# Performance work log

Hardware: AMD Instinct MI355X
Metric: run time of the kernel (lower is better)

## Reference

```python
import jax, jax.numpy as jnp
import numpy as np

N_NODES = 100000
N_EDGES = 1600000
N_CLASS = 45


def gcn_conv(x, W, b, src, dst, ew, n):
    # PyG GCNConv: add self-loops (weight 1), symmetric deg^-1/2 normalization,
    # linear transform, scatter-add aggregation into targets, then bias.
    loops = jnp.arange(n, dtype=src.dtype)
    s = jnp.concatenate([src, loops])
    d = jnp.concatenate([dst, loops])
    w = jnp.concatenate([ew, jnp.ones((n,), ew.dtype)])
    deg = jax.ops.segment_sum(w, d, num_segments=n)          # in-degree (weighted)
    dis = jnp.where(deg > 0, 1.0 / jnp.sqrt(deg), 0.0)      # deg^-1/2, 0 where deg==0
    norm = dis[s] * w * dis[d]                               # [E+n]
    h = x @ W                                                # [n, out]
    out = jax.ops.segment_sum(h[s] * norm[:, None], d, num_segments=n)
    return out + b


def setup_inputs() -> dict:
    key = jax.random.key(0)
    ks = jax.random.split(key, 6)
    x = jax.random.normal(ks[0], (N_NODES, N_CLASS), dtype=jnp.float32)
    edge_src = jax.random.randint(ks[1], (N_EDGES,), 0, N_NODES, dtype=jnp.int64 if jax.config.jax_enable_x64 else jnp.int32).astype(jnp.int32)
    edge_dst = jax.random.randint(ks[2], (N_EDGES,), 0, N_NODES, dtype=jnp.int64 if jax.config.jax_enable_x64 else jnp.int32).astype(jnp.int32)
    edge_w = jax.random.uniform(ks[3], (N_EDGES,), dtype=jnp.float32)
    W1 = jax.random.normal(ks[4], (N_CLASS, 32), dtype=jnp.float32) / np.sqrt(N_CLASS)
    b1 = jnp.zeros((32,), dtype=jnp.float32)
    W2 = jax.random.normal(ks[5], (32, 128), dtype=jnp.float32) / np.sqrt(32.0)
    b2 = jnp.zeros((128,), dtype=jnp.float32)
    return {"x": x, "edge_src": edge_src, "edge_dst": edge_dst, "edge_w": edge_w,
            "W1": W1, "b1": b1, "W2": W2, "b2": b2}


def reference(x, edge_src, edge_dst, edge_w, W1, b1, W2, b2):
    n = x.shape[0]
    h = jnp.tanh(gcn_conv(x, W1, b1, edge_src, edge_dst, edge_w, n))
    return gcn_conv(h, W2, b2, edge_src, edge_dst, edge_w, n)
```

## Files before the change

kernel.cpp:

```cpp
#include <hip/hip_runtime.h>
#include <hip/hip_fp16.h>
#include <math.h>

static constexpr int TPB = 256;
static constexpr int NPB_SHIFT = 8;
static constexpr int BCAP = 5120;
static constexpr int HCAP = 2816;
static constexpr int CSTRIDE = 2 * HCAP;
static constexpr int PCHUNK = 4096;
static constexpr int PF = 16;

__device__ __forceinline__ int p_src(unsigned p) { return (int)(p >> 15); }
__device__ __forceinline__ float p_w(unsigned p) {
  return __half2float(__ushort_as_half((unsigned short)(p & 0x7FFFu)));
}

struct h2x4 { __half2 a, b, c, d; };

__device__ __forceinline__ __half2 shfl_h2(__half2 v, int mask) {
  int b = *reinterpret_cast<int*>(&v);
  int r = __shfl_xor(b, mask, 64);
  return *reinterpret_cast<__half2*>(&r);
}

__global__ void k_partition(const int* __restrict__ src, const int* __restrict__ dst,
                            const float* __restrict__ ew, int* __restrict__ bkcnt,
                            unsigned* __restrict__ ppk, unsigned char* __restrict__ pld,
                            int E, int NB) {
  __shared__ int lh[512];
  __shared__ int lbase[512];
  __shared__ int lcur[512];
  int tid = threadIdx.x;
  long long e0 = (long long)blockIdx.x * PCHUNK;
  int d[PCHUNK / TPB];
  unsigned pk[PCHUNK / TPB];
  for (int t = tid; t < NB; t += TPB) { lh[t] = 0; lcur[t] = 0; }
  __syncthreads();
#pragma unroll
  for (int r = 0; r < PCHUNK / TPB; ++r) {
    long long e = e0 + (long long)r * TPB + tid;
    if (e < E) {
      d[r] = dst[e];
      pk[r] = ((unsigned)src[e] << 15) |
              ((unsigned)__half_as_ushort(__float2half(ew[e])) & 0x7FFFu);
      atomicAdd(&lh[d[r] >> NPB_SHIFT], 1);
    } else {
      d[r] = -1;
    }
  }
  __syncthreads();
  for (int t = tid; t < NB; t += TPB)
    lbase[t] = lh[t] ? (t * BCAP + atomicAdd(&bkcnt[t], lh[t])) : 0;
  __syncthreads();
#pragma unroll
  for (int r = 0; r < PCHUNK / TPB; ++r) {
    if (d[r] >= 0) {
      int b = d[r] >> NPB_SHIFT;
      int pos = atomicAdd(&lcur[b], 1);
      size_t gp = (size_t)lbase[b] + pos;
      ppk[gp] = pk[r];
      pld[gp] = (unsigned char)(d[r] & 255);
    }
  }
}

__global__ void __launch_bounds__(TPB) k_bucket(const unsigned* __restrict__ ppk,
                                                const unsigned char* __restrict__ pld,
                                                const int* __restrict__ bkcnt,
                                                unsigned* __restrict__ csr,
                                                int2* __restrict__ rc,
                                                float* __restrict__ dis,
                                                const float* __restrict__ x,
                                                const float* __restrict__ W1,
                                                __half2* __restrict__ hh, int n) {
  __shared__ float sW[45 * 32];
  __shared__ int lcnt[128];
  __shared__ int lofs[128];
  __shared__ float lsum[128];
  int b = blockIdx.x >> 1;
  int half = blockIdx.x & 1;
  int t = threadIdx.x;
  int beg = b * BCAP;
  int cbeg = b * CSTRIDE + half * HCAP;
  int m = bkcnt[b];
  if (m > BCAP) m = BCAP;
  if (t < 128) { lcnt[t] = 0; lsum[t] = 0.f; }
  for (int i = t; i < 45 * 32; i += TPB) sW[i] = W1[i];
  __syncthreads();
  for (int i = t; i < m; i += TPB) {
    int ld = pld[(size_t)beg + i];
    if ((ld >> 7) == half) atomicAdd(&lcnt[ld & 127], 1);
  }
  __syncthreads();
  int v = (t < 128) ? lcnt[t] : 0;
  if (t < 128) lofs[t] = v;
  __syncthreads();
  for (int off = 1; off < 128; off <<= 1) {
    int tv = (t < 128 && t >= off) ? lofs[t - off] : 0;
    __syncthreads();
    if (t < 128) lofs[t] += tv;
    __syncthreads();
  }
  int gnode = (b << NPB_SHIFT) + half * 128 + t;
  if (t < 128) {
    int ex = lofs[t] - v;
    if (gnode < n) rc[gnode] = make_int2(cbeg + ex, v);
    lcnt[t] = ex;
  }
  __syncthreads();
  for (int i = t; i < m; i += TPB) {
    int ld = pld[(size_t)beg + i];
    if ((ld >> 7) == half) {
      unsigned pk = ppk[(size_t)beg + i];
      int pos = atomicAdd(&lcnt[ld & 127], 1);
      csr[(size_t)cbeg + pos] = pk;
      atomicAdd(&lsum[ld & 127], p_w(pk));
    }
  }
  __syncthreads();
  int ln = t >> 1;
  int jh = t & 1;
  int gnode2 = (b << NPB_SHIFT) + half * 128 + ln;
  if (gnode2 < n) {
    float dsc = rsqrtf(1.0f + lsum[ln]);
    if (jh == 0) dis[gnode2] = dsc;
    float xr[45];
#pragma unroll
    for (int k = 0; k < 45; ++k) xr[k] = x[(size_t)gnode2 * 45 + k];
    __half2* hw = hh + (size_t)gnode2 * 16 + jh * 8;
#pragma unroll
    for (int j2 = 0; j2 < 8; ++j2) {
      int j = jh * 16 + j2 * 2;
      float a0 = 0.f, a1 = 0.f;
#pragma unroll
      for (int k = 0; k < 45; ++k) {
        a0 = fmaf(xr[k], sW[k * 32 + j], a0);
        a1 = fmaf(xr[k], sW[k * 32 + j + 1], a1);
      }
      hw[j2] = __floats2half2_rn(a0 * dsc, a1 * dsc);
    }
  }
}

#define ACC_EDGE(pk, cc0, cc1, cc2, cc3)                                             \
  {                                                                                  \
    h2x4 v = *reinterpret_cast<const h2x4*>(tbl + (size_t)p_src(pk) * 16);           \
    float w = p_w(pk);                                                               \
    float2 f;                                                                        \
    f = __half22float2(v.a); cc0.x = fmaf(w, f.x, cc0.x); cc0.y = fmaf(w, f.y, cc0.y); \
    f = __half22float2(v.b); cc1.x = fmaf(w, f.x, cc1.x); cc1.y = fmaf(w, f.y, cc1.y); \
    f = __half22float2(v.c); cc2.x = fmaf(w, f.x, cc2.x); cc2.y = fmaf(w, f.y, cc2.y); \
    f = __half22float2(v.d); cc3.x = fmaf(w, f.x, cc3.x); cc3.y = fmaf(w, f.y, cc3.y); \
  }

#define GATHER_CORE()                                                                \
  float2 c0 = {0.f, 0.f}, c1 = {0.f, 0.f}, c2 = {0.f, 0.f}, c3 = {0.f, 0.f};        \
  float2 d0 = {0.f, 0.f}, d1 = {0.f, 0.f}, d2 = {0.f, 0.f}, d3 = {0.f, 0.f};        \
  unsigned pr[PF];                                                                   \
  _Pragma("unroll") for (int i = 0; i < PF; ++i) { if (i < m) pr[i] = row[i]; }      \
  _Pragma("unroll") for (int i = 0; i < PF; ++i) {                                   \
    if (i < m) {                                                                     \
      if (i & 1) { ACC_EDGE(pr[i], d0, d1, d2, d3) }                                 \
      else       { ACC_EDGE(pr[i], c0, c1, c2, c3) }                                 \
    }                                                                                \
  }                                                                                  \
  int e = PF;                                                                        \
  for (; e + 3 < m; e += 4) {                                                        \
    unsigned p0 = row[e], p1 = row[e + 1], p2 = row[e + 2], p3 = row[e + 3];         \
    ACC_EDGE(p0, c0, c1, c2, c3)                                                     \
    ACC_EDGE(p1, d0, d1, d2, d3)                                                     \
    ACC_EDGE(p2, c0, c1, c2, c3)                                                     \
    ACC_EDGE(p3, d0, d1, d2, d3)                                                     \
  }                                                                                  \
  for (; e < m; ++e) { unsigned p = row[e]; ACC_EDGE(p, c0, c1, c2, c3) }            \
  c0.x += d0.x; c0.y += d0.y; c1.x += d1.x; c1.y += d1.y;                            \
  c2.x += d2.x; c2.y += d2.y; c3.x += d3.x; c3.y += d3.y;

__global__ void k_gather1(const unsigned* __restrict__ csr, const int2* __restrict__ rc,
                          const float* __restrict__ dis, const __half2* __restrict__ hh,
                          const float* __restrict__ b1, __half2* __restrict__ outv, int n) {
  int gid = blockIdx.x * blockDim.x + threadIdx.x;
  int node = gid >> 2;
  if (node >= n) return;
  int q = (threadIdx.x & 3) * 4;
  int2 r = rc[node];
  const unsigned* row = csr + r.x;
  int m = r.y;
  const __half2* tbl = hh + q;
  GATHER_CORE()
  float dd = dis[node];
  h2x4 own = *reinterpret_cast<const h2x4*>(hh + (size_t)node * 16 + q);
  __half2* op = outv + (size_t)node * 16 + q;
  float2 o0 = __half22float2(own.a), o1 = __half22float2(own.b);
  float2 o2 = __half22float2(own.c), o3 = __half22float2(own.d);
  const float4* bp = reinterpret_cast<const float4*>(b1 + q * 2);
  float4 ba = bp[0], bb = bp[1];
  op[0] = __floats2half2_rn(dd * tanhf(ba.x + dd * (c0.x + o0.x)),
                            dd * tanhf(ba.y + dd * (c0.y + o0.y)));
  op[1] = __floats2half2_rn(dd * tanhf(ba.z + dd * (c1.x + o1.x)),
                            dd * tanhf(ba.w + dd * (c1.y + o1.y)));
  op[2] = __floats2half2_rn(dd * tanhf(bb.x + dd * (c2.x + o2.x)),
                            dd * tanhf(bb.y + dd * (c2.y + o2.y)));
  op[3] = __floats2half2_rn(dd * tanhf(bb.z + dd * (c3.x + o3.x)),
                            dd * tanhf(bb.w + dd * (c3.y + o3.y)));
}

__global__ void k_gather2g(const unsigned* __restrict__ csr, const int2* __restrict__ rc,
                           const float* __restrict__ dis, const __half2* __restrict__ hh,
                           const float* __restrict__ W2, const float* __restrict__ b2,
                           float* __restrict__ out, int n) {
  __shared__ float sW[32 * 128];
  __shared__ float sB[128];
  for (int t = threadIdx.x; t < 32 * 128; t += blockDim.x) sW[t] = W2[t];
  if (threadIdx.x < 128) sB[threadIdx.x] = b2[threadIdx.x];
  __syncthreads();
  int gid = blockIdx.x * blockDim.x + threadIdx.x;
  int node = gid >> 2;
  if (node >= n) return;
  int lq = threadIdx.x & 3;
  int q = lq * 4;
  int2 r = rc[node];
  const unsigned* row = csr + r.x;
  int m = r.y;
  const __half2* tbl = hh + q;
  GATHER_CORE()
  float dd = dis[node];
  h2x4 own = *reinterpret_cast<const h2x4*>(hh + (size_t)node * 16 + q);
  float2 o0 = __half22float2(own.a), o1 = __half22float2(own.b);
  float2 o2 = __half22float2(own.c), o3 = __half22float2(own.d);
  __half2 y0 = __floats2half2_rn(dd * (c0.x + o0.x), dd * (c0.y + o0.y));
  __half2 y1 = __floats2half2_rn(dd * (c1.x + o1.x), dd * (c1.y + o1.y));
  __half2 y2 = __floats2half2_rn(dd * (c2.x + o2.x), dd * (c2.y + o2.y));
  __half2 y3 = __floats2half2_rn(dd * (c3.x + o3.x), dd * (c3.y + o3.y));
  __half2 g1_0 = shfl_h2(y0, 1), g1_1 = shfl_h2(y1, 1), g1_2 = shfl_h2(y2, 1), g1_3 = shfl_h2(y3, 1);
  __half2 g2_0 = shfl_h2(y0, 2), g2_1 = shfl_h2(y1, 2), g2_2 = shfl_h2(y2, 2), g2_3 = shfl_h2(y3, 2);
  __half2 g3_0 = shfl_h2(y0, 3), g3_1 = shfl_h2(y1, 3), g3_2 = shfl_h2(y2, 3), g3_3 = shfl_h2(y3, 3);
  int g4 = lq * 4;
  float4 a[8];
#pragma unroll
  for (int qq = 0; qq < 8; ++qq) a[qq] = *reinterpret_cast<const float4*>(&sB[g4 + qq * 16]);
#define GEMM_GRP(kb, h0, h1, h2v, h3v)                                              \
  {                                                                                 \
    __half2 hv[4] = {h0, h1, h2v, h3v};                                             \
    _Pragma("unroll") for (int ii = 0; ii < 4; ++ii) {                              \
      float2 yv = __half22float2(hv[ii]);                                           \
      const float* w0 = &sW[((kb + ii) * 2) * 128 + g4];                            \
      const float* w1 = &sW[((kb + ii) * 2 + 1) * 128 + g4];                        \
      _Pragma("unroll") for (int qq = 0; qq < 8; ++qq) {                            \
        float4 wa = *reinterpret_cast<const float4*>(w0 + qq * 16);                 \
        float4 wb = *reinterpret_cast<const float4*>(w1 + qq * 16);                 \
        a[qq].x = fmaf(yv.x, wa.x, fmaf(yv.y, wb.x, a[qq].x));                      \
        a[qq].y = fmaf(yv.x, wa.y, fmaf(yv.y, wb.y, a[qq].y));                      \
        a[qq].z = fmaf(yv.x, wa.z, fmaf(yv.y, wb.z, a[qq].z));                      \
        a[qq].w = fmaf(yv.x, wa.w, fmaf(yv.y, wb.w, a[qq].w));                      \
      }                                                                             \
    }                                                                               \
  }
  GEMM_GRP(lq * 4, y0, y1, y2, y3)
  GEMM_GRP((lq ^ 1) * 4, g1_0, g1_1, g1_2, g1_3)
  GEMM_GRP((lq ^ 2) * 4, g2_0, g2_1, g2_2, g2_3)
  GEMM_GRP((lq ^ 3) * 4, g3_0, g3_1, g3_2, g3_3)
#undef GEMM_GRP
  float* op = out + (size_t)node * 128 + g4;
#pragma unroll
  for (int qq = 0; qq < 8; ++qq) *reinterpret_cast<float4*>(op + qq * 16) = a[qq];
}

static inline dim3 gx(long long work) { return dim3((unsigned)((work + TPB - 1) / TPB)); }

extern "C" void kernel_launch(void* const* d_in, const int* in_sizes, int n_in,
                              void* d_out, int out_size, void* d_ws, size_t ws_size,
                              hipStream_t stream) {
  const float* x   = (const float*)d_in[0];
  const int*   src = (const int*)d_in[1];
  const int*   dst = (const int*)d_in[2];
  const float* ew  = (const float*)d_in[3];
  const float* W1  = (const float*)d_in[4];
  const float* b1  = (const float*)d_in[5];
  const float* W2  = (const float*)d_in[6];
  const float* b2  = (const float*)d_in[7];
  float* out = (float*)d_out;

  const int n = in_sizes[0] / 45;
  const int E = in_sizes[1];
  const int NB = (n + 255) >> NPB_SHIFT;

  char* w = (char*)d_ws;
  size_t o = 0;
  auto alloc = [&](size_t bytes) { void* p = w + o; o += ((bytes + 255) & ~(size_t)255); return p; };
  int*           bkcnt = (int*)          alloc((size_t)NB * 4);
  unsigned*      ppk   = (unsigned*)     alloc((size_t)NB * BCAP * 4);
  unsigned char* pld   = (unsigned char*)alloc((size_t)NB * BCAP);
  unsigned*      csr   = (unsigned*)     alloc((size_t)NB * CSTRIDE * 4);
  int2*          rc    = (int2*)         alloc((size_t)n * 8);
  float*         dis   = (float*)        alloc((size_t)n * 4);
  __half2*       hh    = (__half2*)      alloc((size_t)n * 32 * 2);
  __half2*       ag1   = (__half2*)      alloc((size_t)n * 32 * 2);

  const int PB = (E + PCHUNK - 1) / PCHUNK;

  hipMemsetAsync(bkcnt, 0, (size_t)NB * 4, stream);
  k_partition<<<PB, TPB, 0, stream>>>(src, dst, ew, bkcnt, ppk, pld, E, NB);
  k_bucket<<<NB * 2, TPB, 0, stream>>>(ppk, pld, bkcnt, csr, rc, dis, x, W1, hh, n);
  k_gather1<<<gx((long long)n * 4), TPB, 0, stream>>>(csr, rc, dis, hh, b1, ag1, n);
  k_gather2g<<<gx((long long)n * 4), TPB, 0, stream>>>(csr, rc, dis, ag1, W2, b2, out, n);
}
```

Before: 138.8 us.

## Split second-layer aggregation from W2 GEMM into separate register-weight kernel

The fused gather+GEMM kernel for layer 2 is split in two. A templated gather kernel writes the aggregated fp16 features to a new buffer, and a grid-stride GEMM kernel then applies W2 and the bias. The GEMM kernel keeps W2 columns in registers, with each lane owning two output columns and processing two nodes per iteration. This removes the shared-memory weight load per block and the cross-lane shuffles, and lets the output writes coalesce. The cost is an extra kernel launch and a round trip of the 6.4MB intermediate through memory.

Result: slower. 149.5 us (+7.7%).

```diff
diff --git a/kernel.cpp b/kernel.cpp
--- a/kernel.cpp
+++ b/kernel.cpp
@@ -16,12 +16,6 @@
 }
 
 struct h2x4 { __half2 a, b, c, d; };
-
-__device__ __forceinline__ __half2 shfl_h2(__half2 v, int mask) {
-  int b = *reinterpret_cast<int*>(&v);
-  int r = __shfl_xor(b, mask, 64);
-  return *reinterpret_cast<__half2*>(&r);
-}
 
 __global__ void k_partition(const int* __restrict__ src, const int* __restrict__ dst,
                             const float* __restrict__ ew, int* __restrict__ bkcnt,
@@ -176,9 +170,10 @@
   c0.x += d0.x; c0.y += d0.y; c1.x += d1.x; c1.y += d1.y;                            \
   c2.x += d2.x; c2.y += d2.y; c3.x += d3.x; c3.y += d3.y;
 
-__global__ void k_gather1(const unsigned* __restrict__ csr, const int2* __restrict__ rc,
-                          const float* __restrict__ dis, const __half2* __restrict__ hh,
-                          const float* __restrict__ b1, __half2* __restrict__ outv, int n) {
+template <bool TANH>
+__global__ void k_gather(const unsigned* __restrict__ csr, const int2* __restrict__ rc,
+                         const float* __restrict__ dis, const __half2* __restrict__ hh,
+                         const float* __restrict__ b1, __half2* __restrict__ outv, int n) {
   int gid = blockIdx.x * blockDim.x + threadIdx.x;
   int node = gid >> 2;
   if (node >= n) return;
@@ -193,77 +188,70 @@
   __half2* op = outv + (size_t)node * 16 + q;
   float2 o0 = __half22float2(own.a), o1 = __half22float2(own.b);
   float2 o2 = __half22float2(own.c), o3 = __half22float2(own.d);
-  const float4* bp = reinterpret_cast<const float4*>(b1 + q * 2);
-  float4 ba = bp[0], bb = bp[1];
-  op[0] = __floats2half2_rn(dd * tanhf(ba.x + dd * (c0.x + o0.x)),
-                            dd * tanhf(ba.y + dd * (c0.y + o0.y)));
-  op[1] = __floats2half2_rn(dd * tanhf(ba.z + dd * (c1.x + o1.x)),
-                            dd * tanhf(ba.w + dd * (c1.y + o1.y)));
-  op[2] = __floats2half2_rn(dd * tanhf(bb.x + dd * (c2.x + o2.x)),
-                            dd * tanhf(bb.y + dd * (c2.y + o2.y)));
-  op[3] = __floats2half2_rn(dd * tanhf(bb.z + dd * (c3.x + o3.x)),
-                            dd * tanhf(bb.w + dd * (c3.y + o3.y)));
-}
-
-__global__ void k_gather2g(const unsigned* __restrict__ csr, const int2* __restrict__ rc,
-                           const float* __restrict__ dis, const __half2* __restrict__ hh,
-                           const float* __restrict__ W2, const float* __restrict__ b2,
-                           float* __restrict__ out, int n) {
-  __shared__ float sW[32 * 128];
-  __shared__ float sB[128];
-  for (int t = threadIdx.x; t < 32 * 128; t += blockDim.x) sW[t] = W2[t];
-  if (threadIdx.x < 128) sB[threadIdx.x] = b2[threadIdx.x];
-  __syncthreads();
-  int gid = blockIdx.x * blockDim.x + threadIdx.x;
-  int node = gid >> 2;
-  if (node >= n) return;
-  int lq = threadIdx.x & 3;
-  int q = lq * 4;
-  int2 r = rc[node];
-  const unsigned* row = csr + r.x;
-  int m = r.y;
-  const __half2* tbl = hh + q;
-  GATHER_CORE()
-  float dd = dis[node];
-  h2x4 own = *reinterpret_cast<const h2x4*>(hh + (size_t)node * 16 + q);
-  float2 o0 = __half22float2(own.a), o1 = __half22float2(own.b);
-  float2 o2 = __half22float2(own.c), o3 = __half22float2(own.d);
-  __half2 y0 = __floats2half2_rn(dd * (c0.x + o0.x), dd * (c0.y + o0.y));
-  __half2 y1 = __floats2half2_rn(dd * (c1.x + o1.x), dd * (c1.y + o1.y));
-  __half2 y2 = __floats2half2_rn(dd * (c2.x + o2.x), dd * (c2.y + o2.y));
-  __half2 y3 = __floats2half2_rn(dd * (c3.x + o3.x), dd * (c3.y + o3.y));
-  __half2 g1_0 = shfl_h2(y0, 1), g1_1 = shfl_h2(y1, 1), g1_2 = shfl_h2(y2, 1), g1_3 = shfl_h2(y3, 1);
-  __half2 g2_0 = shfl_h2(y0, 2), g2_1 = shfl_h2(y1, 2), g2_2 = shfl_h2(y2, 2), g2_3 = shfl_h2(y3, 2);
-  __half2 g3_0 = shfl_h2(y0, 3), g3_1 = shfl_h2(y1, 3), g3_2 = shfl_h2(y2, 3), g3_3 = shfl_h2(y3, 3);
-  int g4 = lq * 4;
-  float4 a[8];
-#pragma unroll
-  for (int qq = 0; qq < 8; ++qq) a[qq] = *reinterpret_cast<const float4*>(&sB[g4 + qq * 16]);
-#define GEMM_GRP(kb, h0, h1, h2v, h3v)                                              \
-  {                                                                                 \
-    __half2 hv[4] = {h0, h1, h2v, h3v};                                             \
-    _Pragma("unroll") for (int ii = 0; ii < 4; ++ii) {                              \
-      float2 yv = __half22float2(hv[ii]);                                           \
-      const float* w0 = &sW[((kb + ii) * 2) * 128 + g4];                            \
-      const float* w1 = &sW[((kb + ii) * 2 + 1) * 128 + g4];                        \
-      _Pragma("unroll") for (int qq = 0; qq < 8; ++qq) {                            \
-        float4 wa = *reinterpret_cast<const float4*>(w0 + qq * 16);                 \
-        float4 wb = *reinterpret_cast<const float4*>(w1 + qq * 16);                 \
-        a[qq].x = fmaf(yv.x, wa.x, fmaf(yv.y, wb.x, a[qq].x));                      \
-        a[qq].y = fmaf(yv.x, wa.y, fmaf(yv.y, wb.y, a[qq].y));                      \
-        a[qq].z = fmaf(yv.x, wa.z, fmaf(yv.y, wb.z, a[qq].z));                      \
-        a[qq].w = fmaf(yv.x, wa.w, fmaf(yv.y, wb.w, a[qq].w));                      \
-      }                                                                             \
-    }                                                                               \
-  }
-  GEMM_GRP(lq * 4, y0, y1, y2, y3)
-  GEMM_GRP((lq ^ 1) * 4, g1_0, g1_1, g1_2, g1_3)
-  GEMM_GRP((lq ^ 2) * 4, g2_0, g2_1, g2_2, g2_3)
-  GEMM_GRP((lq ^ 3) * 4, g3_0, g3_1, g3_2, g3_3)
-#undef GEMM_GRP
-  float* op = out + (size_t)node * 128 + g4;
-#pragma unroll
-  for (int qq = 0; qq < 8; ++qq) *reinterpret_cast<float4*>(op + qq * 16) = a[qq];
+  if (TANH) {
+    const float4* bp = reinterpret_cast<const float4*>(b1 + q * 2);
+    float4 ba = bp[0], bb = bp[1];
+    op[0] = __floats2half2_rn(dd * tanhf(ba.x + dd * (c0.x + o0.x)),
+                              dd * tanhf(ba.y + dd * (c0.y + o0.y)));
+    op[1] = __floats2half2_rn(dd * tanhf(ba.z + dd * (c1.x + o1.x)),
+                              dd * tanhf(ba.w + dd * (c1.y + o1.y)));
+    op[2] = __floats2half2_rn(dd * tanhf(bb.x + dd * (c2.x + o2.x)),
+                              dd * tanhf(bb.y + dd * (c2.y + o2.y)));
+    op[3] = __floats2half2_rn(dd * tanhf(bb.z + dd * (c3.x + o3.x)),
+                              dd * tanhf(bb.w + dd * (c3.y + o3.y)));
+  } else {
+    op[0] = __floats2half2_rn(dd * (c0.x + o0.x), dd * (c0.y + o0.y));
+    op[1] = __floats2half2_rn(dd * (c1.x + o1.x), dd * (c1.y + o1.y));
+    op[2] = __floats2half2_rn(dd * (c2.x + o2.x), dd * (c2.y + o2.y));
+    op[3] = __floats2half2_rn(dd * (c3.x + o3.x), dd * (c3.y + o3.y));
+  }
+}
+
+__global__ void k_gemm2r(const __half2* __restrict__ y, const float* __restrict__ W2,
+                         const float* __restrict__ b2, float* __restrict__ out, int n) {
+  int lane = threadIdx.x & 63;
+  int wid = (blockIdx.x * blockDim.x + threadIdx.x) >> 6;
+  int nw = (gridDim.x * blockDim.x) >> 6;
+  int c0 = lane * 2;
+  float wr0[32], wr1[32];
+#pragma unroll
+  for (int k = 0; k < 32; ++k) {
+    float2 wv = *reinterpret_cast<const float2*>(W2 + k * 128 + c0);
+    wr0[k] = wv.x; wr1[k] = wv.y;
+  }
+  float2 bb = *reinterpret_cast<const float2*>(b2 + c0);
+
+#define GEMM_NODE(node, ox, oy)                                                      \
+  {                                                                                  \
+    const h2x4* yr = reinterpret_cast<const h2x4*>(y + (size_t)(node) * 16);         \
+    h2x4 yv[4] = {yr[0], yr[1], yr[2], yr[3]};                                       \
+    _Pragma("unroll") for (int g = 0; g < 4; ++g) {                                  \
+      __half2 hs[4] = {yv[g].a, yv[g].b, yv[g].c, yv[g].d};                          \
+      _Pragma("unroll") for (int i = 0; i < 4; ++i) {                                \
+        float2 f = __half22float2(hs[i]);                                            \
+        ox = fmaf(f.x, wr0[g * 8 + i * 2], ox);                                      \
+        oy = fmaf(f.x, wr1[g * 8 + i * 2], oy);                                      \
+        ox = fmaf(f.y, wr0[g * 8 + i * 2 + 1], ox);                                  \
+        oy = fmaf(f.y, wr1[g * 8 + i * 2 + 1], oy);                                  \
+      }                                                                              \
+    }                                                                                \
+  }
+
+  int node = wid * 2;
+  int stride = nw * 2;
+  for (; node + 1 < n; node += stride) {
+    float a0 = bb.x, a1 = bb.y, b0 = bb.x, b1v = bb.y;
+    GEMM_NODE(node, a0, a1)
+    GEMM_NODE(node + 1, b0, b1v)
+    *reinterpret_cast<float2*>(out + (size_t)node * 128 + c0) = make_float2(a0, a1);
+    *reinterpret_cast<float2*>(out + (size_t)(node + 1) * 128 + c0) = make_float2(b0, b1v);
+  }
+  if (node < n) {
+    float a0 = bb.x, a1 = bb.y;
+    GEMM_NODE(node, a0, a1)
+    *reinterpret_cast<float2*>(out + (size_t)node * 128 + c0) = make_float2(a0, a1);
+  }
+#undef GEMM_NODE
 }
 
 static inline dim3 gx(long long work) { return dim3((unsigned)((work + TPB - 1) / TPB)); }
@@ -296,12 +284,14 @@
   float*         dis   = (float*)        alloc((size_t)n * 4);
   __half2*       hh    = (__half2*)      alloc((size_t)n * 32 * 2);
   __half2*       ag1   = (__half2*)      alloc((size_t)n * 32 * 2);
+  __half2*       yb    = (__half2*)      alloc((size_t)n * 32 * 2);
 
   const int PB = (E + PCHUNK - 1) / PCHUNK;
 
   hipMemsetAsync(bkcnt, 0, (size_t)NB * 4, stream);
   k_partition<<<PB, TPB, 0, stream>>>(src, dst, ew, bkcnt, ppk, pld, E, NB);
   k_bucket<<<NB * 2, TPB, 0, stream>>>(ppk, pld, bkcnt, csr, rc, dis, x, W1, hh, n);
-  k_gather1<<<gx((long long)n * 4), TPB, 0, stream>>>(csr, rc, dis, hh, b1, ag1, n);
-  k_gather2g<<<gx((long long)n * 4), TPB, 0, stream>>>(csr, rc, dis, ag1, W2, b2, out, n);
-}
+  k_gather<true><<<gx((long long)n * 4), TPB, 0, stream>>>(csr, rc, dis, hh, b1, ag1, n);
+  k_gather<false><<<gx((long long)n * 4), TPB, 0, stream>>>(csr, rc, dis, ag1, b1, yb, n);
+  k_gemm2r<<<1024, TPB, 0, stream>>>(yb, W2, b2, out, n);
+}
```
